# Optimization experiments

Hardware: AMD Instinct MI355X
Metric: run time of the kernel (lower is better)

Reference implementation:

```python
import jax, jax.numpy as jnp
import numpy as np

N, HW, L = 16, 3136, 64
C_IN, C_OUT, D = 256, 512, 256


def setup_inputs() -> dict:
    key = jax.random.key(0)
    ks = jax.random.split(key, 8)
    # xavier-normal-ish scale for weights
    def xav(k, shape):
        fan_in, fan_out = shape[1], shape[0]
        std = (2.0 / (fan_in + fan_out)) ** 0.5
        return jax.random.normal(k, shape, dtype=jnp.float32) * std
    return {
        "x": jax.random.normal(ks[0], (N, HW, C_IN), dtype=jnp.float32),
        "t": jax.random.normal(ks[1], (N, L, D), dtype=jnp.float32),
        "W1": xav(ks[2], (D, C_IN)),      # linear1 weight (out,in), no bias
        "W2": xav(ks[3], (D, D)),         # linear2 weight, no bias
        "W3": xav(ks[4], (C_OUT, D)),     # linear3 weight
        "b3": jnp.zeros((C_OUT,), dtype=jnp.float32),
        "Wd": xav(ks[5], (C_OUT, C_IN)),  # downsample weight
        "bd": jnp.zeros((C_OUT,), dtype=jnp.float32),
    }


def reference(x, t, W1, W2, W3, b3, Wd, bd):
    # x: (N, HW, C_in), t: (N, L, D)
    x_q = jnp.einsum("npc,dc->npd", x, W1)          # (N, HW, D)
    t_q = jnp.einsum("nld,ed->nle", t, W2)          # (N, L, D)
    a = jnp.einsum("npd,nld->npl", x_q, t_q)        # unscaled QK^T (N, HW, L)
    a = jax.nn.softmax(a, axis=2)
    t3 = jnp.einsum("nld,od->nlo", t, W3) + b3      # (N, L, C_out)
    av = jnp.einsum("npl,nlo->npo", a, t3)          # (N, HW, C_out)
    x_ds = jnp.einsum("npc,oc->npo", x, Wd) + bd    # downsample residual
    return x_ds + av
```

## Files before the change

### kernel.cpp

```cpp
#include <hip/hip_runtime.h>


typedef unsigned short u16;
using half8 = __attribute__((ext_vector_type(8))) _Float16;
using f32x4 = __attribute__((ext_vector_type(4))) float;

__device__ __forceinline__ u16 f2h(float f) {
  _Float16 h = (_Float16)f;
  union { _Float16 h; u16 u; } cv; cv.h = h;
  return cv.u;
}

__device__ __forceinline__ f32x4 mfma16(half8 a, half8 b, f32x4 c) {
  return __builtin_amdgcn_mfma_f32_16x16x32_f16(a, b, c, 0, 0, 0);
}

__global__ __launch_bounds__(256) void prep_kernel(
    const float* __restrict__ W1, const float* __restrict__ W2,
    const float* __restrict__ W3, const float* __restrict__ Wd,
    const float* __restrict__ t,
    u16* __restrict__ W3f, u16* __restrict__ Wdf, u16* __restrict__ tf,
    u16* __restrict__ Gtf) {
  int b = blockIdx.x, k = threadIdx.x;
  if (b < 2048) {
    const float* src; u16* dst; int row;
    if (b < 512)       { src = W3; dst = W3f; row = b; }
    else if (b < 1024) { src = Wd; dst = Wdf; row = b - 512; }
    else               { src = t;  dst = tf;  row = b - 1024; }
    float v = src[(size_t)row*256 + k];
    int flat = ((row >> 4)*8 + (k >> 5))*512 + ((k >> 3) & 3)*128 + (row & 15)*8 + (k & 7);
    dst[flat] = f2h(v);
  } else {
    int c = b - 2048;
    float g = 0.f;
    #pragma unroll 8
    for (int d = 0; d < 256; ++d)
      g = fmaf(W1[d*256 + c], W2[d*256 + k], g);
    int flat = ((c >> 4)*8 + (k >> 5))*512 + ((k >> 3) & 3)*128 + (c & 15)*8 + (k & 7);
    Gtf[flat] = f2h(g);
  }
}

__global__ __launch_bounds__(256) void mt_t3_kernel(
    const u16* __restrict__ tf, const u16* __restrict__ Gtf,
    const u16* __restrict__ W3f, const float* __restrict__ b3,
    u16* __restrict__ mtf, u16* __restrict__ t3f) {
  const int tid = threadIdx.x, w = tid >> 6, lane = tid & 63;
  const int quad = lane >> 4, l16 = lane & 15;
  const int b = blockIdx.x;

  if (b < 64) {
    const int n = b >> 2, eb = b & 3;
    const int gc = eb*4 + w;
    f32x4 acc[4];
    #pragma unroll
    for (int mt = 0; mt < 4; ++mt) acc[mt] = (f32x4){0.f, 0.f, 0.f, 0.f};
    #pragma unroll
    for (int kc = 0; kc < 8; ++kc) {
      half8 bf = *(const half8*)(Gtf + (gc*8 + kc)*512 + lane*8);
      #pragma unroll
      for (int mt = 0; mt < 4; ++mt) {
        half8 a = *(const half8*)(tf + ((n*4 + mt)*8 + kc)*512 + lane*8);
        acc[mt] = mfma16(a, bf, acc[mt]);
      }
    }
    #pragma unroll
    for (int mt = 0; mt < 4; ++mt)
      #pragma unroll
      for (int r = 0; r < 4; ++r) {
        int flat = ((n*4 + mt)*8 + eb*2 + (w >> 1))*512
                 + ((w & 1)*2 + (l16 >> 3))*128 + (quad*4 + r)*8 + (l16 & 7);
        mtf[flat] = f2h(acc[mt][r]);
      }
  } else {
    const int b2 = b - 64;
    const int n = b2 >> 3, ob = b2 & 7;
    const int gW3 = ob*4 + w;
    f32x4 acc[4];
    #pragma unroll
    for (int nt = 0; nt < 4; ++nt) acc[nt] = (f32x4){0.f, 0.f, 0.f, 0.f};
    #pragma unroll
    for (int kc = 0; kc < 8; ++kc) {
      half8 a = *(const half8*)(W3f + (gW3*8 + kc)*512 + lane*8);
      #pragma unroll
      for (int nt = 0; nt < 4; ++nt) {
        half8 bf = *(const half8*)(tf + ((n*4 + nt)*8 + kc)*512 + lane*8);
        acc[nt] = mfma16(a, bf, acc[nt]);
      }
    }
    #pragma unroll
    for (int nt = 0; nt < 4; ++nt)
      #pragma unroll
      for (int r = 0; r < 4; ++r) {
        int o = ob*64 + w*16 + quad*4 + r;
        int flat = ((n*32 + ob*4 + w)*2 + (nt >> 1))*512
                 + ((nt & 1)*2 + (l16 >> 3))*128 + (quad*4 + r)*8 + (l16 & 7);
        t3f[flat] = f2h(acc[nt][r] + b3[o]);
      }
  }
}

__global__ __launch_bounds__(512, 4) void main_kernel(
    const float* __restrict__ x, const u16* __restrict__ Wdf,
    const u16* __restrict__ mtf, const u16* __restrict__ t3f,
    const float* __restrict__ bd, float* __restrict__ out) {
  __shared__ __attribute__((aligned(16))) char smem[44032];
  u16* xs = (u16*)smem;
  u16* aw = (u16*)(smem + 33792);
  float* parts = (float*)(smem + 43008);

  const int bid = blockIdx.x;
  const int n  = bid / 49;
  const int pt = bid - n*49;
  const int m0 = pt * 64;
  const int tid = threadIdx.x, w = tid >> 6, lane = tid & 63;
  const int quad = lane >> 4, l16 = lane & 15;
  const int rg = w & 3;
  const int lp = w >> 2;

  float bias[4];
  #pragma unroll
  for (int ot = 0; ot < 4; ++ot) bias[ot] = bd[w*64 + ot*16 + l16];

  {
    const float4* xg = (const float4*)(x + (size_t)(n*3136 + m0)*256);
    #pragma unroll
    for (int it = 0; it < 8; ++it) {
      int idx = it*512 + tid;
      int r = idx >> 6, c4 = idx & 63;
      float4 v = xg[idx];
      ushort4 u;
      u.x = f2h(v.x); u.y = f2h(v.y); u.z = f2h(v.z); u.w = f2h(v.w);
      *(ushort4*)(&xs[r*264 + c4*4]) = u;
    }
  }
  __syncthreads();

  f32x4 acc2[2];
  acc2[0] = (f32x4){0.f, 0.f, 0.f, 0.f};
  acc2[1] = (f32x4){0.f, 0.f, 0.f, 0.f};
  #pragma unroll
  for (int kc = 0; kc < 8; ++kc) {
    half8 a = *(const half8*)(&xs[(rg*16 + l16)*264 + kc*32 + quad*8]);
    #pragma unroll
    for (int j = 0; j < 2; ++j) {
      half8 bf = *(const half8*)(mtf + ((size_t)(n*4 + lp*2 + j)*8 + kc)*512 + lane*8);
      acc2[j] = mfma16(a, bf, acc2[j]);
    }
  }

  float mx_[4], ps_[4], e0_[4], e1_[4];
  #pragma unroll
  for (int r = 0; r < 4; ++r) {
    float s0 = acc2[0][r], s1 = acc2[1][r];
    float mx = fmaxf(s0, s1);
    #pragma unroll
    for (int off = 8; off >= 1; off >>= 1) mx = fmaxf(mx, __shfl_xor(mx, off, 64));
    float e0 = __expf(s0 - mx), e1 = __expf(s1 - mx);
    float ps = e0 + e1;
    #pragma unroll
    for (int off = 8; off >= 1; off >>= 1) ps += __shfl_xor(ps, off, 64);
    mx_[r] = mx; ps_[r] = ps; e0_[r] = e0; e1_[r] = e1;
    if (l16 == 0) {
      int row = rg*16 + quad*4 + r;
      parts[(row*2 + lp)*2]     = mx;
      parts[(row*2 + lp)*2 + 1] = ps;
    }
  }
  __syncthreads();

  #pragma unroll
  for (int r = 0; r < 4; ++r) {
    int row = rg*16 + quad*4 + r;
    float mxo = parts[(row*2 + (1 - lp))*2];
    float pso = parts[(row*2 + (1 - lp))*2 + 1];
    float g  = fmaxf(mx_[r], mxo);
    float sA = __expf(mx_[r] - g), sB = __expf(mxo - g);
    float inv = 1.0f / (ps_[r]*sA + pso*sB);
    float scl = sA * inv;
    aw[row*72 + (lp*2)*16 + l16]     = f2h(e0_[r]*scl);
    aw[row*72 + (lp*2 + 1)*16 + l16] = f2h(e1_[r]*scl);
  }
  __syncthreads();

  f32x4 acc[4][4];
  #pragma unroll
  for (int mt = 0; mt < 4; ++mt)
    #pragma unroll
    for (int ot = 0; ot < 4; ++ot) acc[mt][ot] = (f32x4){0.f, 0.f, 0.f, 0.f};
  #pragma unroll
  for (int kc = 0; kc < 8; ++kc) {
    half8 a[4];
    #pragma unroll
    for (int mt = 0; mt < 4; ++mt)
      a[mt] = *(const half8*)(&xs[(mt*16 + l16)*264 + kc*32 + quad*8]);
    #pragma unroll
    for (int ot = 0; ot < 4; ++ot) {
      half8 bf = *(const half8*)(Wdf + ((size_t)(w*4 + ot)*8 + kc)*512 + lane*8);
      #pragma unroll
      for (int mt = 0; mt < 4; ++mt) acc[mt][ot] = mfma16(a[mt], bf, acc[mt][ot]);
    }
  }
  #pragma unroll
  for (int kc3 = 0; kc3 < 2; ++kc3) {
    half8 a[4];
    #pragma unroll
    for (int mt = 0; mt < 4; ++mt)
      a[mt] = *(const half8*)(&aw[(mt*16 + l16)*72 + kc3*32 + quad*8]);
    #pragma unroll
    for (int ot = 0; ot < 4; ++ot) {
      half8 bf = *(const half8*)(t3f + ((size_t)(n*32 + w*4 + ot)*2 + kc3)*512 + lane*8);
      #pragma unroll
      for (int mt = 0; mt < 4; ++mt) acc[mt][ot] = mfma16(a[mt], bf, acc[mt][ot]);
    }
  }
  __syncthreads();

  float* sc = (float*)smem + w*1088;
  #pragma unroll
  for (int mt = 0; mt < 4; ++mt) {
    #pragma unroll
    for (int ot = 0; ot < 4; ++ot)
      #pragma unroll
      for (int r = 0; r < 4; ++r)
        sc[(quad*4 + r)*68 + ot*16 + l16] = acc[mt][ot][r] + bias[ot];
    #pragma unroll
    for (int i = 0; i < 4; ++i) {
      float4 v = *(float4*)&sc[(i*4 + quad)*68 + l16*4];
      *(float4*)&out[(size_t)(n*3136 + m0 + mt*16 + i*4 + quad)*512 + w*64 + l16*4] = v;
    }
  }
}

extern "C" void kernel_launch(void* const* d_in, const int* in_sizes, int n_in,
                              void* d_out, int out_size, void* d_ws, size_t ws_size,
                              hipStream_t stream) {
  const float* x  = (const float*)d_in[0];
  const float* t  = (const float*)d_in[1];
  const float* W1 = (const float*)d_in[2];
  const float* W2 = (const float*)d_in[3];
  const float* W3 = (const float*)d_in[4];
  const float* b3 = (const float*)d_in[5];
  const float* Wd = (const float*)d_in[6];
  const float* bd = (const float*)d_in[7];
  float* out = (float*)d_out;

  char* ws = (char*)d_ws;
  u16* W3f = (u16*)(ws + 0);
  u16* Wdf = (u16*)(ws + 262144);
  u16* tf  = (u16*)(ws + 524288);
  u16* Gtf = (u16*)(ws + 1048576);
  u16* mtf = (u16*)(ws + 1179648);
  u16* t3f = (u16*)(ws + 1703936);

  hipLaunchKernelGGL(prep_kernel, dim3(2304), dim3(256), 0, stream,
                     W1, W2, W3, Wd, t, W3f, Wdf, tf, Gtf);
  hipLaunchKernelGGL(mt_t3_kernel, dim3(192), dim3(256), 0, stream,
                     tf, Gtf, W3f, b3, mtf, t3f);
  hipLaunchKernelGGL(main_kernel, dim3(784), dim3(512), 0, stream,
                     x, Wdf, mtf, t3f, bd, out);
}
```

Baseline: 205.7 us.

## Split main kernel output columns into two halves to cut accumulator registers

The main kernel's 4x4 accumulator tile per wave is split into two passes of 4x2. The first half of the downsample GEMM is interleaved with the QK^T score MFMAs before the softmax, and the second half runs afterward. Each half is staged through a new dedicated per-wave LDS scratch region, so the final __syncthreads before output is no longer needed. This lowers register pressure and overlaps downsample work with the softmax phase, at the cost of more LDS per block, which may limit occupancy, and of reloading the x fragments and the aw tile twice. The prep kernel's unroll factor is also raised from 8 to 16.

```diff
diff --git a/kernel.cpp b/kernel.cpp
--- a/kernel.cpp
+++ b/kernel.cpp
@@ -33,7 +33,7 @@
   } else {
     int c = b - 2048;
     float g = 0.f;
-    #pragma unroll 8
+    #pragma unroll 16
     for (int d = 0; d < 256; ++d)
       g = fmaf(W1[d*256 + c], W2[d*256 + k], g);
     int flat = ((c >> 4)*8 + (k >> 5))*512 + ((k >> 3) & 3)*128 + (c & 15)*8 + (k & 7);
@@ -104,10 +104,11 @@
     const float* __restrict__ x, const u16* __restrict__ Wdf,
     const u16* __restrict__ mtf, const u16* __restrict__ t3f,
     const float* __restrict__ bd, float* __restrict__ out) {
-  __shared__ __attribute__((aligned(16))) char smem[44032];
+  __shared__ __attribute__((aligned(16))) char smem[62464];
   u16* xs = (u16*)smem;
   u16* aw = (u16*)(smem + 33792);
   float* parts = (float*)(smem + 43008);
+  float* scb = (float*)(smem + 44032);
 
   const int bid = blockIdx.x;
   const int n  = bid / 49;
@@ -139,13 +140,27 @@
   f32x4 acc2[2];
   acc2[0] = (f32x4){0.f, 0.f, 0.f, 0.f};
   acc2[1] = (f32x4){0.f, 0.f, 0.f, 0.f};
+  f32x4 acc[4][2];
+  #pragma unroll
+  for (int mt = 0; mt < 4; ++mt)
+    #pragma unroll
+    for (int ot = 0; ot < 2; ++ot) acc[mt][ot] = (f32x4){0.f, 0.f, 0.f, 0.f};
   #pragma unroll
   for (int kc = 0; kc < 8; ++kc) {
-    half8 a = *(const half8*)(&xs[(rg*16 + l16)*264 + kc*32 + quad*8]);
+    half8 a[4];
+    #pragma unroll
+    for (int mt = 0; mt < 4; ++mt)
+      a[mt] = *(const half8*)(&xs[(mt*16 + l16)*264 + kc*32 + quad*8]);
     #pragma unroll
     for (int j = 0; j < 2; ++j) {
       half8 bf = *(const half8*)(mtf + ((size_t)(n*4 + lp*2 + j)*8 + kc)*512 + lane*8);
-      acc2[j] = mfma16(a, bf, acc2[j]);
+      acc2[j] = mfma16(a[rg], bf, acc2[j]);
+    }
+    #pragma unroll
+    for (int ot = 0; ot < 2; ++ot) {
+      half8 bf = *(const half8*)(Wdf + ((size_t)(w*4 + ot)*8 + kc)*512 + lane*8);
+      #pragma unroll
+      for (int mt = 0; mt < 4; ++mt) acc[mt][ot] = mfma16(a[mt], bf, acc[mt][ot]);
     }
   }
 
@@ -183,11 +198,40 @@
   }
   __syncthreads();
 
-  f32x4 acc[4][4];
+  #pragma unroll
+  for (int kc3 = 0; kc3 < 2; ++kc3) {
+    half8 a3[4];
+    #pragma unroll
+    for (int mt = 0; mt < 4; ++mt)
+      a3[mt] = *(const half8*)(&aw[(mt*16 + l16)*72 + kc3*32 + quad*8]);
+    #pragma unroll
+    for (int ot = 0; ot < 2; ++ot) {
+      half8 bf = *(const half8*)(t3f + ((size_t)(n*32 + w*4 + ot)*2 + kc3)*512 + lane*8);
+      #pragma unroll
+      for (int mt = 0; mt < 4; ++mt) acc[mt][ot] = mfma16(a3[mt], bf, acc[mt][ot]);
+    }
+  }
+
+  float* sc = scb + w*576;
+  #pragma unroll
+  for (int mt = 0; mt < 4; ++mt) {
+    #pragma unroll
+    for (int ot = 0; ot < 2; ++ot)
+      #pragma unroll
+      for (int r = 0; r < 4; ++r)
+        sc[(quad*4 + r)*36 + ot*16 + l16] = acc[mt][ot][r] + bias[ot];
+    #pragma unroll
+    for (int shot = 0; shot < 2; ++shot) {
+      int row = shot*8 + (lane >> 3);
+      float4 v = *(float4*)&sc[row*36 + (lane & 7)*4];
+      *(float4*)&out[(size_t)(n*3136 + m0 + mt*16 + row)*512 + w*64 + (lane & 7)*4] = v;
+    }
+  }
+
   #pragma unroll
   for (int mt = 0; mt < 4; ++mt)
     #pragma unroll
-    for (int ot = 0; ot < 4; ++ot) acc[mt][ot] = (f32x4){0.f, 0.f, 0.f, 0.f};
+    for (int ot = 0; ot < 2; ++ot) acc[mt][ot] = (f32x4){0.f, 0.f, 0.f, 0.f};
   #pragma unroll
   for (int kc = 0; kc < 8; ++kc) {
     half8 a[4];
@@ -195,39 +239,37 @@
     for (int mt = 0; mt < 4; ++mt)
       a[mt] = *(const half8*)(&xs[(mt*16 + l16)*264 + kc*32 + quad*8]);
     #pragma unroll
-    for (int ot = 0; ot < 4; ++ot) {
-      half8 bf = *(const half8*)(Wdf + ((size_t)(w*4 + ot)*8 + kc)*512 + lane*8);
+    for (int ot = 0; ot < 2; ++ot) {
+      half8 bf = *(const half8*)(Wdf + ((size_t)(w*4 + 2 + ot)*8 + kc)*512 + lane*8);
       #pragma unroll
       for (int mt = 0; mt < 4; ++mt) acc[mt][ot] = mfma16(a[mt], bf, acc[mt][ot]);
     }
   }
   #pragma unroll
   for (int kc3 = 0; kc3 < 2; ++kc3) {
-    half8 a[4];
-    #pragma unroll
-    for (int mt = 0; mt < 4; ++mt)
-      a[mt] = *(const half8*)(&aw[(mt*16 + l16)*72 + kc3*32 + quad*8]);
-    #pragma unroll
-    for (int ot = 0; ot < 4; ++ot) {
-      half8 bf = *(const half8*)(t3f + ((size_t)(n*32 + w*4 + ot)*2 + kc3)*512 + lane*8);
-      #pragma unroll
-      for (int mt = 0; mt < 4; ++mt) acc[mt][ot] = mfma16(a[mt], bf, acc[mt][ot]);
-    }
-  }
-  __syncthreads();
-
-  float* sc = (float*)smem + w*1088;
+    half8 a3[4];
+    #pragma unroll
+    for (int mt = 0; mt < 4; ++mt)
+      a3[mt] = *(const half8*)(&aw[(mt*16 + l16)*72 + kc3*32 + quad*8]);
+    #pragma unroll
+    for (int ot = 0; ot < 2; ++ot) {
+      half8 bf = *(const half8*)(t3f + ((size_t)(n*32 + w*4 + 2 + ot)*2 + kc3)*512 + lane*8);
+      #pragma unroll
+      for (int mt = 0; mt < 4; ++mt) acc[mt][ot] = mfma16(a3[mt], bf, acc[mt][ot]);
+    }
+  }
   #pragma unroll
   for (int mt = 0; mt < 4; ++mt) {
     #pragma unroll
-    for (int ot = 0; ot < 4; ++ot)
+    for (int ot = 0; ot < 2; ++ot)
       #pragma unroll
       for (int r = 0; r < 4; ++r)
-        sc[(quad*4 + r)*68 + ot*16 + l16] = acc[mt][ot][r] + bias[ot];
-    #pragma unroll
-    for (int i = 0; i < 4; ++i) {
-      float4 v = *(float4*)&sc[(i*4 + quad)*68 + l16*4];
-      *(float4*)&out[(size_t)(n*3136 + m0 + mt*16 + i*4 + quad)*512 + w*64 + l16*4] = v;
+        sc[(quad*4 + r)*36 + ot*16 + l16] = acc[mt][ot][r] + bias[2 + ot];
+    #pragma unroll
+    for (int shot = 0; shot < 2; ++shot) {
+      int row = shot*8 + (lane >> 3);
+      float4 v = *(float4*)&sc[row*36 + (lane & 7)*4];
+      *(float4*)&out[(size_t)(n*3136 + m0 + mt*16 + row)*512 + w*64 + 32 + (lane & 7)*4] = v;
     }
   }
 }
```

Measured after the change: 279.2 us. 35.7% more time.
